# Kernel tuning notes

Hardware: AMD Instinct MI355X
Metric: run time of the kernel (lower is better)

The kernel has to match this reference:

```python
import jax, jax.numpy as jnp
import numpy as np

B, S, E = 4, 4096, 512
DK, DV = 64, 64


def setup_inputs() -> dict:
    key = jax.random.key(0)
    ks = jax.random.split(key, 7)
    s_e = 1.0 / np.sqrt(E)
    return {
        "embedding_matrix": jax.random.normal(ks[0], (B, S, E), dtype=jnp.float32),
        # torch Linear init ~ U(-1/sqrt(in), 1/sqrt(in)); stored here as [in, out]
        "Wq_w": jax.random.uniform(ks[1], (E, DK), jnp.float32, -s_e, s_e),
        "Wq_b": jax.random.uniform(ks[2], (DK,), jnp.float32, -s_e, s_e),
        "Wk_w": jax.random.uniform(ks[3], (E, DK), jnp.float32, -s_e, s_e),
        "Wk_b": jax.random.uniform(ks[4], (DK,), jnp.float32, -s_e, s_e),
        "Wv_w": jax.random.uniform(ks[5], (E, DV), jnp.float32, -s_e, s_e),
        "Wv_b": jax.random.uniform(ks[6], (DV,), jnp.float32, -s_e, s_e),
    }


def reference(embedding_matrix, Wq_w, Wq_b, Wk_w, Wk_b, Wv_w, Wv_b):
    # Single-head causal attention, faithful to the torch module (mask=True).
    Q = embedding_matrix @ Wq_w + Wq_b            # [B, S, DK]
    K = embedding_matrix @ Wk_w + Wk_b            # [B, S, DK]
    V = embedding_matrix @ Wv_w + Wv_b            # [B, S, DV]
    dk = K.shape[-1]
    scores = jnp.einsum('bqd,bkd->bqk', Q, K) / jnp.sqrt(jnp.asarray(dk, Q.dtype))
    seq_len = scores.shape[-1]
    causal = jnp.tril(jnp.ones((seq_len, seq_len), dtype=bool))  # keep lower-tri
    scores = jnp.where(causal[None, :, :], scores, -jnp.inf)
    attn = jax.nn.softmax(scores.astype(jnp.float32), axis=-1)
    return jnp.einsum('bqk,bkd->bqd', attn, V)
```

## Files before the change

### kernel.cpp

```cpp
#include <hip/hip_runtime.h>
#include <hip/hip_bf16.h>

#define B_ 4
#define S_ 4096
#define E_ 512
#define D_ 64

typedef float  f32x4  __attribute__((ext_vector_type(4)));
typedef float  f32x16 __attribute__((ext_vector_type(16)));
typedef short  s16x8  __attribute__((ext_vector_type(8)));

__device__ inline short f2bf(float f){
  unsigned u = __builtin_bit_cast(unsigned, f);
  u += 0x7fffu + ((u >> 16) & 1u);
  return (short)(u >> 16);
}
__device__ inline unsigned bfpack(float a, float b){
  unsigned ua = __builtin_bit_cast(unsigned, a);
  unsigned ub = __builtin_bit_cast(unsigned, b);
  ua += 0x7fffu + ((ua >> 16) & 1u);
  ub += 0x7fffu + ((ub >> 16) & 1u);
  return (ua >> 16) | (ub & 0xffff0000u);
}
__device__ inline float ex2(float x){ return __builtin_amdgcn_exp2f(x); }

#define QSCALE 0.18033688f


__global__ __launch_bounds__(256) void prep_kernel(const float* __restrict__ Wq,
                                                   const float* __restrict__ Wk,
                                                   const float* __restrict__ Wv,
                                                   short* __restrict__ Wtf){
  int o = blockIdx.x * 256 + threadIdx.x;
  int cbi = o >> 13;
  int l   = (o >> 3) & 63;
  int j   = o & 7;
  int kk  = (o >> 9) & 15;
  int n = cbi * 16 + (l & 15);
  int k = kk * 32 + (l >> 4) * 8 + j;
  const float* W = (n < 64) ? Wq : (n < 128 ? Wk : Wv);
  float v = W[k * 64 + (n & 63)];
  if (n < 64) v *= QSCALE;
  Wtf[o] = f2bf(v);
}

__global__ __launch_bounds__(256) void proj_kernel(const float* __restrict__ X,
                                                   const short* __restrict__ Wtf,
                                                   const float* __restrict__ bq,
                                                   const float* __restrict__ bk,
                                                   const float* __restrict__ bv,
                                                   short* __restrict__ Qf,
                                                   short* __restrict__ Kf,
                                                   short* __restrict__ Vf){
  __shared__ short Xs[1024 * 8];
  __shared__ short Os[16][136];
  __shared__ short OsT[64][24];

  const int tid = threadIdx.x;
  const int l = tid & 63, w = tid >> 6;
  const int c = l & 15,  g = l >> 4;
  const int r0 = blockIdx.x * 16;
  const int t  = (r0 >> 5) & 127;
  const int h  = (r0 >> 4) & 1;
  const int b  = r0 >> 12;

#pragma unroll
  for (int i = 0; i < 4; i++){
    int ch  = i * 256 + tid;
    int row = ch >> 6, gr = ch & 63;
    const float* xp = X + (size_t)(r0 + row) * E_ + gr * 8;
    f32x4 a0 = *reinterpret_cast<const f32x4*>(xp);
    f32x4 a1 = *reinterpret_cast<const f32x4*>(xp + 4);
    s16x8 hv;
#pragma unroll
    for (int q = 0; q < 4; q++){ hv[q] = f2bf(a0[q]); hv[4+q] = f2bf(a1[q]); }
    *reinterpret_cast<s16x8*>(&Xs[(row * 64 + (gr ^ (row & 7))) * 8]) = hv;
  }
  __syncthreads();

  f32x4 acc[3];
#pragma unroll
  for (int j = 0; j < 3; j++) acc[j] = (f32x4){0.f,0.f,0.f,0.f};

  for (int kk = 0; kk < 16; kk++){
    s16x8 af = *reinterpret_cast<const s16x8*>(&Xs[(c * 64 + ((kk * 4 + g) ^ (c & 7))) * 8]);
#pragma unroll
    for (int j = 0; j < 3; j++){
      int cbi = w * 3 + j;
      s16x8 bf = *reinterpret_cast<const s16x8*>(Wtf + (((size_t)(cbi * 16 + kk)) << 9) + (l << 3));
      acc[j] = __builtin_amdgcn_mfma_f32_16x16x32_bf16(af, bf, acc[j], 0, 0, 0);
    }
  }

#pragma unroll
  for (int j = 0; j < 3; j++){
    int cbi = w * 3 + j;
    int d = ((cbi & 3) << 4) + c;
    if (cbi < 8){
      float bias = (cbi < 4) ? bq[d] * QSCALE : bk[d];
      int col = (cbi < 4) ? d : (64 + d);
#pragma unroll
      for (int r = 0; r < 4; r++) Os[g * 4 + r][col] = f2bf(acc[j][r] + bias);
    } else {
      float bias = bv[d];
      union { unsigned long long u; short s[4]; } pk;
#pragma unroll
      for (int r = 0; r < 4; r++) pk.s[r] = f2bf(acc[j][r] + bias);
      *reinterpret_cast<unsigned long long*>(&OsT[d][g * 4]) = pk.u;
    }
  }
  __syncthreads();

  const size_t tbase = ((size_t)(b * 128 + t)) << 11;
  {
    int q = tid & 127;
    int N = q >> 5, hd = (q >> 4) & 1, lo16 = q & 15;
    int d0 = N * 16 + hd * 8;
    int col = (tid < 128) ? d0 : (64 + d0);
    s16x8 vv = *reinterpret_cast<const s16x8*>(&Os[lo16][col]);
    short* dst = (tid < 128 ? Qf : Kf) + tbase + N * 512 + hd * 256 + (h * 16 + lo16) * 8;
    *reinterpret_cast<s16x8*>(dst) = vv;
  }
  if (tid < 128){
    int hf = tid >> 6, ht = (tid >> 5) & 1, dl = tid & 31;
    s16x8 vv = *reinterpret_cast<const s16x8*>(&OsT[hf * 32 + dl][ht * 8]);
    short* dst = Vf + tbase + (h + 2 * hf) * 512 + ht * 256 + dl * 8;
    *reinterpret_cast<s16x8*>(dst) = vv;
  }
}

__global__ __launch_bounds__(512, 4) void attn_kernel(const short* __restrict__ Qf,
                                                      const short* __restrict__ Kf,
                                                      const short* __restrict__ Vf,
                                                      float* __restrict__ out){
  __shared__ float accw[8][32][64];
  __shared__ float lw[8][32];

  const int tid = threadIdx.x;
  const int w  = tid >> 6;
  const int l  = tid & 63;
  const int lo = l & 31, hi = l >> 5;
  const int bid = blockIdx.x;
  const int b  = bid & 3;
  const int jj = (bid >> 2) & 63;
  const int t  = (bid >> 8) ? jj : 127 - jj;
  const int q0 = t << 5;

  const short* qb = Qf + (((size_t)(b * 128 + t)) << 11) + (l << 3);
  s16x8 qf0 = *reinterpret_cast<const s16x8*>(qb);
  s16x8 qf1 = *reinterpret_cast<const s16x8*>(qb + 512);
  s16x8 qf2 = *reinterpret_cast<const s16x8*>(qb + 1024);
  s16x8 qf3 = *reinterpret_cast<const s16x8*>(qb + 1536);

  float ls = 0.f;
  f32x16 acc0, acc1;
#pragma unroll
  for (int r = 0; r < 16; r++){ acc0[r] = 0.f; acc1[r] = 0.f; }

  const int nkt = t + 1;
  for (int kt = w; kt < nkt; kt += 8){
    const int k0 = kt << 5;
    const short* kb = Kf + (((size_t)(b * 128 + kt)) << 11) + (l << 3);
    s16x8 kf0 = *reinterpret_cast<const s16x8*>(kb);
    s16x8 kf1 = *reinterpret_cast<const s16x8*>(kb + 512);
    s16x8 kf2 = *reinterpret_cast<const s16x8*>(kb + 1024);
    s16x8 kf3 = *reinterpret_cast<const s16x8*>(kb + 1536);
    const short* vb = Vf + (((size_t)(b * 128 + kt)) << 11) + (l << 3);
    s16x8 v00 = *reinterpret_cast<const s16x8*>(vb);
    s16x8 v01 = *reinterpret_cast<const s16x8*>(vb + 512);
    s16x8 v10 = *reinterpret_cast<const s16x8*>(vb + 1024);
    s16x8 v11 = *reinterpret_cast<const s16x8*>(vb + 1536);

    f32x16 s;
#pragma unroll
    for (int r = 0; r < 16; r++) s[r] = 0.f;
    s = __builtin_amdgcn_mfma_f32_32x32x16_bf16(kf0, qf0, s, 0, 0, 0);
    s = __builtin_amdgcn_mfma_f32_32x32x16_bf16(kf1, qf1, s, 0, 0, 0);
    s = __builtin_amdgcn_mfma_f32_32x32x16_bf16(kf2, qf2, s, 0, 0, 0);
    s = __builtin_amdgcn_mfma_f32_32x32x16_bf16(kf3, qf3, s, 0, 0, 0);

    if (k0 == q0){
#pragma unroll
      for (int r = 0; r < 16; r++){
        int key = (r & 3) + ((r >> 2) << 3) + (hi << 2);
        if (key > lo) s[r] = -1e30f;
      }
    }

#pragma unroll
    for (int r = 0; r < 16; r++) s[r] = ex2(s[r]);

    float y0 = s[0]+s[1], y1 = s[2]+s[3], y2 = s[4]+s[5], y3 = s[6]+s[7];
    float y4 = s[8]+s[9], y5 = s[10]+s[11], y6 = s[12]+s[13], y7 = s[14]+s[15];
    float rs = ((y0+y1)+(y2+y3)) + ((y4+y5)+(y6+y7));
    rs += __shfl_xor(rs, 32);
    ls += rs;

    unsigned pk0 = bfpack(s[0], s[1]),   pk1 = bfpack(s[2], s[3]);
    unsigned pk2 = bfpack(s[4], s[5]),   pk3 = bfpack(s[6], s[7]);
    unsigned pk4 = bfpack(s[8], s[9]),   pk5 = bfpack(s[10], s[11]);
    unsigned pk6 = bfpack(s[12], s[13]), pk7 = bfpack(s[14], s[15]);

    unsigned sd0 = hi ? pk0 : pk2, sd1 = hi ? pk1 : pk3;
    unsigned rv0 = (unsigned)__shfl_xor((int)sd0, 32);
    unsigned rv1 = (unsigned)__shfl_xor((int)sd1, 32);
    union { s16x8 v; unsigned u[4]; } A0, A1;
    A0.u[0] = hi ? rv0 : pk0; A0.u[1] = hi ? rv1 : pk1;
    A0.u[2] = hi ? pk2 : rv0; A0.u[3] = hi ? pk3 : rv1;

    unsigned sd2 = hi ? pk4 : pk6, sd3 = hi ? pk5 : pk7;
    unsigned rv2 = (unsigned)__shfl_xor((int)sd2, 32);
    unsigned rv3 = (unsigned)__shfl_xor((int)sd3, 32);
    A1.u[0] = hi ? rv2 : pk4; A1.u[1] = hi ? rv3 : pk5;
    A1.u[2] = hi ? pk6 : rv2; A1.u[3] = hi ? pk7 : rv3;

    acc0 = __builtin_amdgcn_mfma_f32_32x32x16_bf16(A0.v, v00, acc0, 0, 0, 0);
    acc0 = __builtin_amdgcn_mfma_f32_32x32x16_bf16(A1.v, v01, acc0, 0, 0, 0);
    acc1 = __builtin_amdgcn_mfma_f32_32x32x16_bf16(A0.v, v10, acc1, 0, 0, 0);
    acc1 = __builtin_amdgcn_mfma_f32_32x32x16_bf16(A1.v, v11, acc1, 0, 0, 0);
  }

#pragma unroll
  for (int r = 0; r < 16; r++){
    int q = (r & 3) + ((r >> 2) << 3) + (hi << 2);
    accw[w][q][lo]      = acc0[r];
    accw[w][q][32 + lo] = acc1[r];
  }
  if (hi == 0) lw[w][lo] = ls;
  __syncthreads();

  {
    int q  = tid >> 4;
    int dg = (tid & 15) << 2;
    float L = 0.f;
    f32x4 o = (f32x4){0.f,0.f,0.f,0.f};
#pragma unroll
    for (int j = 0; j < 8; j++){
      L += lw[j][q];
      f32x4 a = *reinterpret_cast<const f32x4*>(&accw[j][q][dg]);
      o += a;
    }
    f32x4 res = o * (1.f / L);
    *reinterpret_cast<f32x4*>(out + ((size_t)((b << 12) + q0 + q)) * D_ + dg) = res;
  }
}

extern "C" void kernel_launch(void* const* d_in, const int* in_sizes, int n_in,
                              void* d_out, int out_size, void* d_ws, size_t ws_size,
                              hipStream_t stream){
  const float* X  = (const float*)d_in[0];
  const float* Wq = (const float*)d_in[1];
  const float* bq = (const float*)d_in[2];
  const float* Wk = (const float*)d_in[3];
  const float* bk = (const float*)d_in[4];
  const float* Wv = (const float*)d_in[5];
  const float* bv = (const float*)d_in[6];
  float* out = (float*)d_out;

  char* base = (char*)d_ws;
  short* Wtf = (short*)(base);
  short* Qf  = (short*)(base + 196608);
  short* Kf  = (short*)(base + 196608 + 2097152);
  short* Vf  = (short*)(base + 196608 + 2 * 2097152);

  prep_kernel<<<384, 256, 0, stream>>>(Wq, Wk, Wv, Wtf);
  proj_kernel<<<1024, 256, 0, stream>>>(X, Wtf, bq, bk, bv, Qf, Kf, Vf);
  attn_kernel<<<512, 512, 0, stream>>>(Qf, Kf, Vf, out);
}
```

Baseline: 111.1 us.

## Process 32 rows per projection block to reuse weight fragments across two MFMAs

The projection kernel now handles 32 rows of X per block instead of 16, halving the grid to 512 blocks. Each weight fragment loaded from global memory feeds two MFMAs, one per 16-row half, which halves weight traffic per output row. Shared memory becomes a 32 KB dynamic buffer that is reused for the output staging tiles after an extra barrier. The write-out maps each thread to one full 32-row tile segment for Q, K and V. The trade-off is fewer blocks, more shared memory per block and an added sync, which may lower occupancy and latency hiding.

```diff
diff --git a/kernel.cpp b/kernel.cpp
--- a/kernel.cpp
+++ b/kernel.cpp
@@ -52,20 +52,18 @@
                                                    short* __restrict__ Qf,
                                                    short* __restrict__ Kf,
                                                    short* __restrict__ Vf){
-  __shared__ short Xs[1024 * 8];
-  __shared__ short Os[16][136];
-  __shared__ short OsT[64][24];
+  extern __shared__ short buf[];
+  short* Xs = buf;
 
   const int tid = threadIdx.x;
   const int l = tid & 63, w = tid >> 6;
   const int c = l & 15,  g = l >> 4;
-  const int r0 = blockIdx.x * 16;
-  const int t  = (r0 >> 5) & 127;
-  const int h  = (r0 >> 4) & 1;
-  const int b  = r0 >> 12;
-
-#pragma unroll
-  for (int i = 0; i < 4; i++){
+  const int t  = blockIdx.x & 127;
+  const int b  = blockIdx.x >> 7;
+  const int r0 = blockIdx.x * 32;
+
+#pragma unroll
+  for (int i = 0; i < 8; i++){
     int ch  = i * 256 + tid;
     int row = ch >> 6, gr = ch & 63;
     const float* xp = X + (size_t)(r0 + row) * E_ + gr * 8;
@@ -78,19 +76,27 @@
   }
   __syncthreads();
 
-  f32x4 acc[3];
-#pragma unroll
-  for (int j = 0; j < 3; j++) acc[j] = (f32x4){0.f,0.f,0.f,0.f};
+  f32x4 acc[3][2];
+#pragma unroll
+  for (int j = 0; j < 3; j++)
+#pragma unroll
+    for (int hf = 0; hf < 2; hf++) acc[j][hf] = (f32x4){0.f,0.f,0.f,0.f};
 
   for (int kk = 0; kk < 16; kk++){
-    s16x8 af = *reinterpret_cast<const s16x8*>(&Xs[(c * 64 + ((kk * 4 + g) ^ (c & 7))) * 8]);
+    s16x8 af0 = *reinterpret_cast<const s16x8*>(&Xs[(c * 64        + ((kk * 4 + g) ^ (c & 7))) * 8]);
+    s16x8 af1 = *reinterpret_cast<const s16x8*>(&Xs[((16 + c) * 64 + ((kk * 4 + g) ^ (c & 7))) * 8]);
 #pragma unroll
     for (int j = 0; j < 3; j++){
       int cbi = w * 3 + j;
       s16x8 bf = *reinterpret_cast<const s16x8*>(Wtf + (((size_t)(cbi * 16 + kk)) << 9) + (l << 3));
-      acc[j] = __builtin_amdgcn_mfma_f32_16x16x32_bf16(af, bf, acc[j], 0, 0, 0);
-    }
-  }
+      acc[j][0] = __builtin_amdgcn_mfma_f32_16x16x32_bf16(af0, bf, acc[j][0], 0, 0, 0);
+      acc[j][1] = __builtin_amdgcn_mfma_f32_16x16x32_bf16(af1, bf, acc[j][1], 0, 0, 0);
+    }
+  }
+  __syncthreads();
+
+  short* Os  = buf;
+  short* OsT = buf + 32 * 136;
 
 #pragma unroll
   for (int j = 0; j < 3; j++){
@@ -100,32 +106,35 @@
       float bias = (cbi < 4) ? bq[d] * QSCALE : bk[d];
       int col = (cbi < 4) ? d : (64 + d);
 #pragma unroll
-      for (int r = 0; r < 4; r++) Os[g * 4 + r][col] = f2bf(acc[j][r] + bias);
+      for (int hf = 0; hf < 2; hf++)
+#pragma unroll
+        for (int r = 0; r < 4; r++)
+          Os[(hf * 16 + g * 4 + r) * 136 + col] = f2bf(acc[j][hf][r] + bias);
     } else {
       float bias = bv[d];
-      union { unsigned long long u; short s[4]; } pk;
-#pragma unroll
-      for (int r = 0; r < 4; r++) pk.s[r] = f2bf(acc[j][r] + bias);
-      *reinterpret_cast<unsigned long long*>(&OsT[d][g * 4]) = pk.u;
+#pragma unroll
+      for (int hf = 0; hf < 2; hf++){
+        union { unsigned long long u; short s[4]; } pk;
+#pragma unroll
+        for (int r = 0; r < 4; r++) pk.s[r] = f2bf(acc[j][hf][r] + bias);
+        *reinterpret_cast<unsigned long long*>(&OsT[d * 48 + hf * 16 + g * 4]) = pk.u;
+      }
     }
   }
   __syncthreads();
 
   const size_t tbase = ((size_t)(b * 128 + t)) << 11;
   {
-    int q = tid & 127;
-    int N = q >> 5, hd = (q >> 4) & 1, lo16 = q & 15;
-    int d0 = N * 16 + hd * 8;
-    int col = (tid < 128) ? d0 : (64 + d0);
-    s16x8 vv = *reinterpret_cast<const s16x8*>(&Os[lo16][col]);
-    short* dst = (tid < 128 ? Qf : Kf) + tbase + N * 512 + hd * 256 + (h * 16 + lo16) * 8;
-    *reinterpret_cast<s16x8*>(dst) = vv;
-  }
-  if (tid < 128){
-    int hf = tid >> 6, ht = (tid >> 5) & 1, dl = tid & 31;
-    s16x8 vv = *reinterpret_cast<const s16x8*>(&OsT[hf * 32 + dl][ht * 8]);
-    short* dst = Vf + tbase + (h + 2 * hf) * 512 + ht * 256 + dl * 8;
-    *reinterpret_cast<s16x8*>(dst) = vv;
+    int N  = tid >> 6;
+    int ll = tid & 63;
+    int lo = ll & 31, hi = ll >> 5;
+    s16x8 vq = *reinterpret_cast<const s16x8*>(&Os[lo * 136 + N * 16 + hi * 8]);
+    *reinterpret_cast<s16x8*>(Qf + tbase + N * 512 + ll * 8) = vq;
+    s16x8 vk = *reinterpret_cast<const s16x8*>(&Os[lo * 136 + 64 + N * 16 + hi * 8]);
+    *reinterpret_cast<s16x8*>(Kf + tbase + N * 512 + ll * 8) = vk;
+    int kh = N & 1, half = N >> 1;
+    s16x8 vv = *reinterpret_cast<const s16x8*>(&OsT[(half * 32 + lo) * 48 + kh * 16 + hi * 8]);
+    *reinterpret_cast<s16x8*>(Vf + tbase + N * 512 + ll * 8) = vv;
   }
 }
 
@@ -264,6 +273,6 @@
   short* Vf  = (short*)(base + 196608 + 2 * 2097152);
 
   prep_kernel<<<384, 256, 0, stream>>>(Wq, Wk, Wv, Wtf);
-  proj_kernel<<<1024, 256, 0, stream>>>(X, Wtf, bq, bk, bv, Qf, Kf, Vf);
+  proj_kernel<<<512, 256, 32768, stream>>>(X, Wtf, bq, bk, bv, Qf, Kf, Vf);
   attn_kernel<<<512, 512, 0, stream>>>(Qf, Kf, Vf, out);
 }
```

Measured after the change: 113.8 us. 2.4% more time.
